# Performance work log

Hardware: AMD Instinct MI355X
Metric: run time of the kernel (lower is better)

## Reference

```python
import jax, jax.numpy as jnp
import numpy as np

B, N, D, H = 512, 200, 128, 8
DH = D // H
CLIP = 10.0
NEG = -1e9


def setup_inputs():
    ks = jax.random.split(jax.random.key(0), 10)
    s = 1.0 / float(np.sqrt(D))
    f32 = jnp.float32
    return {
        "x": jax.random.normal(ks[0], (2, B, N, N), f32),
        "rf": jax.random.uniform(ks[1], (B, 2), f32),
        "node_embeddings": jax.random.normal(ks[2], (B, N, D), f32),
        "graph_embedding": jax.random.normal(ks[3], (B, D), f32),
        "Wk1_w": jax.random.normal(ks[4], (D, D), f32) * s,
        "Wk1_b": jnp.zeros((D,), f32),
        "Wv_w": jax.random.normal(ks[5], (D, D), f32) * s,
        "Wk2_w": jax.random.normal(ks[6], (D, D), f32) * s,
        "Wout_w": jax.random.normal(ks[7], (D, D), f32) * s,
        "Wq_w": jax.random.normal(ks[8], (D, D + 2), f32) * s,
        "init_node": jnp.zeros((D,), f32),
    }


def _forward(x, rf, node_embeddings, Wk1_w, Wk1_b, Wv_w, Wk2_w, Wout_w, Wq_w, init_node):
    # static projections (compute_static)
    K1 = node_embeddings @ Wk1_w.T + Wk1_b  # [B,N,D]
    V = node_embeddings @ Wv_w.T
    K2 = node_embeddings @ Wk2_w.T
    K1h = K1.reshape(B, N, H, DH).transpose(0, 2, 1, 3)  # [B,H,N,DH]
    Vh = V.reshape(B, N, H, DH).transpose(0, 2, 1, 3)
    barange = jnp.arange(B)
    narange = jnp.arange(N)

    def step(carry, _):
        mask, ctx, end = carry  # mask [B,N] bool, ctx [B,2+D], end [B] bool
        Q1 = ctx @ Wq_w.T  # [B,D]  (Wq_step)
        qh = Q1.reshape(B, H, DH)
        scores = jnp.einsum('bhd,bhnd->bhn', qh, K1h) / jnp.sqrt(jnp.float32(DH))
        scores = jnp.where(mask[:, None, :], NEG, scores)
        attn = jax.nn.softmax(scores, axis=-1)
        mha = jnp.einsum('bhn,bhnd->bhd', attn, Vh).reshape(B, D)
        Q2 = mha @ Wout_w.T  # [B,D]
        logits = CLIP * jnp.tanh(jnp.einsum('bd,bnd->bn', Q2, K2) / jnp.sqrt(jnp.float32(D)))
        logits = jnp.where(mask, NEG, logits)
        log_p = jax.nn.log_softmax(logits, axis=-1)  # [B,N]
        nxt = jnp.argmax(log_p, axis=-1)  # greedy decode (deterministic)
        nxt = jnp.where(end, nxt, 0)  # once node 0 chosen, stay at 0
        cur_emb = node_embeddings[barange, nxt]  # [B,D]
        end = end & (nxt != 0)
        mask = mask | (narange[None, :] == nxt[:, None])
        ctx = jnp.concatenate([rf, cur_emb], axis=1)
        return (mask, ctx, end), (log_p, nxt)

    ctx0 = jnp.concatenate([rf, jnp.broadcast_to(init_node, (B, D))], axis=1)
    carry0 = (jnp.zeros((B, N), bool), ctx0, jnp.ones((B,), bool))
    _, (log_ps, tours) = jax.lax.scan(step, carry0, None, length=N)
    log_ps = log_ps.transpose(1, 0, 2)  # [B,N,N]
    pi = tours.T  # [B,N]

    # get_cost
    index = jnp.argmax(pi == 0, axis=1)  # first occurrence of stop node 0
    steps_mask = narange[None, :] < index[:, None]
    cols = pi * steps_mask
    sol = jnp.zeros((B, N), jnp.float32).at[barange[:, None], cols].set(1.0)
    f1 = jnp.einsum('bn,bnm,bm->b', sol, x[0], sol)[:, None, None]  # [B,1,1]
    f2 = jnp.einsum('bn,bnm,bm->b', sol, x[1], sol)[:, None, None]
    cost = -(f1 * rf[0, 0] + f2 * rf[0, 1]).squeeze()  # [B]

    # log-likelihood of tour, weighted by solution membership
    chosen = jnp.take_along_axis(log_ps, pi[:, :, None], axis=2)[:, :, 0]  # [B,N]
    w = jnp.take_along_axis(sol, pi, axis=1)
    ll = jnp.sum(chosen * w, axis=1)  # [B]
    return cost, f1, f2, ll, pi


def reference(x, rf, node_embeddings, graph_embedding, Wk1_w, Wk1_b, Wv_w, Wk2_w, Wout_w, Wq_w, init_node):
    return _forward(x, rf, node_embeddings, Wk1_w, Wk1_b, Wv_w, Wk2_w, Wout_w, Wq_w, init_node)
```

## Files before the change

### kernel.cpp

```cpp
#include <hip/hip_runtime.h>
#include <math.h>

#define NEGV (-1e9f)

#define OUT_F   0l
#define M_F     52428800l
#define QR_F    (M_F + 65536l)
#define QI_F    (QR_F + 65536l)
#define SOL_F   (QI_F + 65536l)
#define WS_FLOATS (SOL_F + 102400l)

typedef float f32x4 __attribute__((ext_vector_type(4)));

#define DPPF(x, ctrl, oldv) __int_as_float(__builtin_amdgcn_update_dpp( \
      __float_as_int(oldv), __float_as_int(x), ctrl, 0xF, 0xF, false))

__device__ __forceinline__ float wave_max(float x) {
  x = fmaxf(x, DPPF(x, 0x111, -INFINITY));
  x = fmaxf(x, DPPF(x, 0x112, -INFINITY));
  x = fmaxf(x, DPPF(x, 0x114, -INFINITY));
  x = fmaxf(x, DPPF(x, 0x118, -INFINITY));
  x = fmaxf(x, DPPF(x, 0x142, -INFINITY));
  x = fmaxf(x, DPPF(x, 0x143, -INFINITY));
  return __int_as_float(__builtin_amdgcn_readlane(__float_as_int(x), 63));
}
__device__ __forceinline__ float wave_sum(float x) {
  x = x + DPPF(x, 0x111, 0.f);
  x = x + DPPF(x, 0x112, 0.f);
  x = x + DPPF(x, 0x114, 0.f);
  x = x + DPPF(x, 0x118, 0.f);
  x = x + DPPF(x, 0x142, 0.f);
  x = x + DPPF(x, 0x143, 0.f);
  return __int_as_float(__builtin_amdgcn_readlane(__float_as_int(x), 63));
}

__global__ __launch_bounds__(256)
void build_M(const float* __restrict__ Wk1, const float* __restrict__ Wv,
             const float* __restrict__ Wk2, const float* __restrict__ Wout,
             const float* __restrict__ Wq, float* __restrict__ Mbuf) {
  int g = blockIdx.x * 256 + threadIdx.x;
  int j = g >> 9, c = g & 511;
  float val;
  if (c < 128) {
    val = Wk1[c * 128 + j];
  } else if (c < 256) {
    val = Wv[(c - 128) * 128 + j];
  } else if (c < 384) {
    int d = c - 256;
    float s = 0.f;
    for (int e = 0; e < 128; ++e) s += Wk2[e * 128 + j] * Wout[e * 128 + d];
    val = s;
  } else {
    val = Wq[(c - 384) * 130 + 2 + j];
  }
  Mbuf[j * 512 + c] = val;
}

__global__ __launch_bounds__(256)
void build_Q(const float* __restrict__ rf, const float* __restrict__ Wq,
             const float* __restrict__ initn, float* __restrict__ QR,
             float* __restrict__ QI) {
  int g = blockIdx.x * 256 + threadIdx.x;
  int b = g >> 7, d = g & 127;
  float qr = Wq[d * 130 + 0] * rf[b * 2 + 0] + Wq[d * 130 + 1] * rf[b * 2 + 1];
  float qi = qr;
  for (int j = 0; j < 128; ++j) qi += Wq[d * 130 + 2 + j] * initn[j];
  QR[g] = qr;
  QI[g] = qi;
}

__global__ __launch_bounds__(256)
void gemm_static(const float* __restrict__ emb, const float* __restrict__ Mbuf,
                 const float* __restrict__ bk1, const float* __restrict__ QR,
                 float* __restrict__ OUT) {
  int bid = blockIdx.x;
  int lo = bid & 7, hi = bid >> 3;
  int rt = lo + 8 * (hi % 200);
  int ct = hi / 200;
  int r0 = rt * 64, c0 = ct * 64;
  int t = threadIdx.x, ty = t >> 4, tx = t & 15;
  int row0 = r0 + ty * 4;
  int col  = c0 + tx * 4;
  float acc[4][4] = {};
  const float* mp = Mbuf + col;
  for (int kb = 0; kb < 32; ++kb) {
    int k = kb * 4;
    float4 b0 = *(const float4*)(mp + (long)(k + 0) * 512);
    float4 b1 = *(const float4*)(mp + (long)(k + 1) * 512);
    float4 b2 = *(const float4*)(mp + (long)(k + 2) * 512);
    float4 b3 = *(const float4*)(mp + (long)(k + 3) * 512);
    float bm[4][4] = {{b0.x,b0.y,b0.z,b0.w},{b1.x,b1.y,b1.z,b1.w},
                      {b2.x,b2.y,b2.z,b2.w},{b3.x,b3.y,b3.z,b3.w}};
    #pragma unroll
    for (int rr = 0; rr < 4; ++rr) {
      float4 a4 = *(const float4*)(emb + (long)(row0 + rr) * 128 + k);
      float av[4] = {a4.x, a4.y, a4.z, a4.w};
      #pragma unroll
      for (int i = 0; i < 4; ++i)
        #pragma unroll
        for (int cc = 0; cc < 4; ++cc)
          acc[rr][cc] += av[i] * bm[i][cc];
    }
  }
  float badd[4] = {0.f, 0.f, 0.f, 0.f};
  if (c0 < 128) {
    #pragma unroll
    for (int cc = 0; cc < 4; ++cc) badd[cc] = bk1[col + cc];
  }
  #pragma unroll
  for (int rr = 0; rr < 4; ++rr) {
    int row = row0 + rr;
    float v[4];
    #pragma unroll
    for (int cc = 0; cc < 4; ++cc) v[cc] = acc[rr][cc] + badd[cc];
    if (col >= 384) {
      int bb = row / 200;
      #pragma unroll
      for (int cc = 0; cc < 4; ++cc) v[cc] += QR[bb * 128 + (col - 384) + cc];
    }
    float4 v4; v4.x = v[0]; v4.y = v[1]; v4.z = v[2]; v4.w = v[3];
    *(float4*)(OUT + (long)row * 512 + col) = v4;
  }
}

__global__ void init_ctr(int* __restrict__ c) { *c = 0; }

__global__ __attribute__((amdgpu_flat_work_group_size(512, 512), amdgpu_waves_per_eu(2, 2)))
void decode512(const float* __restrict__ OUT, const float* __restrict__ QI,
               int* __restrict__ ctr, float* __restrict__ sol,
               float* __restrict__ out) {
  __shared__ __align__(16) float qall[201 * 128];
  __shared__ float sc[1600];
  __shared__ __align__(16) float mhal[128];
  __shared__ float lg[200];
  __shared__ int bci, bsel;

  const int t = threadIdx.x;
  const int lane = t & 63, wave = t >> 6;
  const int o = t >> 2, r4 = t & 3;
  const int mn = t >> 1, half = t & 1;
  const int vst  = (r4 == 0) ? 0 : (r4 == 1 ? 48 : (r4 == 2 ? 100 : 152));
  const bool mid = (r4 == 1) || (r4 == 2);

  float kreg[64], ureg[64], vreg[52];

  for (;;) {
    if (t == 0) bsel = atomicAdd(ctr, 1);
    __syncthreads();
    const int b = bsel;
    if (b >= 512) break;
    const float* outb = OUT + (long)b * 200 * 512;

    for (int f = t; f < 25728; f += 512) {
      int row = f >> 7, d = f & 127;
      qall[f] = (row < 200) ? outb[row * 512 + 384 + d] : QI[b * 128 + d];
    }
    #pragma unroll
    for (int k = 0; k < 4; ++k) {
      int n = lane + 64 * k;
      if (n < 200) {
        const float* kp = outb + n * 512 + wave * 16;
        #pragma unroll
        for (int c = 0; c < 4; ++c)
          *(f32x4*)&kreg[k * 16 + c * 4] = *(const f32x4*)(kp + c * 4);
      } else {
        #pragma unroll
        for (int c = 0; c < 16; ++c) kreg[k * 16 + c] = 0.f;
      }
    }
    if (t < 400) {
      const float* up = outb + mn * 512 + 256 + 64 * half;
      #pragma unroll
      for (int c = 0; c < 16; ++c)
        *(f32x4*)&ureg[c * 4] = *(const f32x4*)(up + c * 4);
    }
    {
      const float* vp = outb + 128 + o;
      #pragma unroll
      for (int i = 0; i < 48; ++i) vreg[i] = vp[(vst + i) * 512];
      vreg[48] = mid ? vp[(vst + 48) * 512] : 0.f;
      vreg[49] = mid ? vp[(vst + 49) * 512] : 0.f;
      vreg[50] = mid ? vp[(vst + 50) * 512] : 0.f;
      vreg[51] = mid ? vp[(vst + 51) * 512] : 0.f;
    }

    int cur = 200;
    int mk = 0;
    bool cmb = false;
    bool live = true, picked0 = false;
    float llsum = 0.f, chose = 0.f;

    __syncthreads();

    for (int st = 0; st < 200; ++st) {
      {
        const float* qb = qall + cur * 128 + wave * 16;
        f32x4 q0 = *(const f32x4*)(qb + 0);
        f32x4 q1 = *(const f32x4*)(qb + 4);
        f32x4 q2 = *(const f32x4*)(qb + 8);
        f32x4 q3 = *(const f32x4*)(qb + 12);
        float sv[4];
        float mx = -INFINITY;
        #pragma unroll
        for (int k = 0; k < 4; ++k) {
          int n = lane + 64 * k;
          float s = -INFINITY;
          if (n < 200) {
            float a = q0[0] * kreg[k * 16 + 0];
            a += q0[1] * kreg[k * 16 + 1];
            a += q0[2] * kreg[k * 16 + 2];
            a += q0[3] * kreg[k * 16 + 3];
            a += q1[0] * kreg[k * 16 + 4];
            a += q1[1] * kreg[k * 16 + 5];
            a += q1[2] * kreg[k * 16 + 6];
            a += q1[3] * kreg[k * 16 + 7];
            a += q2[0] * kreg[k * 16 + 8];
            a += q2[1] * kreg[k * 16 + 9];
            a += q2[2] * kreg[k * 16 + 10];
            a += q2[3] * kreg[k * 16 + 11];
            a += q3[0] * kreg[k * 16 + 12];
            a += q3[1] * kreg[k * 16 + 13];
            a += q3[2] * kreg[k * 16 + 14];
            a += q3[3] * kreg[k * 16 + 15];
            s = a * 0.25f;
            if (mk & (1 << k)) s = NEGV;
          }
          sv[k] = s;
          mx = fmaxf(mx, s);
        }
        float vmax = wave_max(mx);
        float ls = 0.f;
        #pragma unroll
        for (int k = 0; k < 4; ++k) { sv[k] = expf(sv[k] - vmax); ls += sv[k]; }
        ls = wave_sum(ls);
        #pragma unroll
        for (int k = 0; k < 4; ++k) {
          int n = lane + 64 * k;
          if (n < 200) sc[wave * 200 + n] = sv[k] / ls;
        }
      }

      {
        const float* ap = sc + wave * 200 + vst;
        float ac[4] = {0.f, 0.f, 0.f, 0.f};
        #pragma unroll
        for (int c = 0; c < 12; ++c) {
          f32x4 av = *(const f32x4*)(ap + c * 4);
          float s = av[0] * vreg[c * 4 + 0];
          s += av[1] * vreg[c * 4 + 1];
          s += av[2] * vreg[c * 4 + 2];
          s += av[3] * vreg[c * 4 + 3];
          ac[c & 3] += s;
        }
        if (mid) {
          f32x4 av = *(const f32x4*)(ap + 48);
          float s = av[0] * vreg[48];
          s += av[1] * vreg[49]; s += av[2] * vreg[50]; s += av[3] * vreg[51];
          ac[0] += s;
        }
        float a = (ac[0] + ac[1]) + (ac[2] + ac[3]);
        a += DPPF(a, 0xB1, 0.f);
        a += DPPF(a, 0x4E, 0.f);
        if (r4 == 0) mhal[o] = a;
      }
      __syncthreads();

      if (t < 400) {
        float ac[4] = {0.f, 0.f, 0.f, 0.f};
        #pragma unroll
        for (int c = 0; c < 16; ++c) {
          f32x4 mh = *(const f32x4*)&mhal[64 * half + c * 4];
          float s = mh[0] * ureg[c * 4 + 0];
          s += mh[1] * ureg[c * 4 + 1];
          s += mh[2] * ureg[c * 4 + 2];
          s += mh[3] * ureg[c * 4 + 3];
          ac[c & 3] += s;
        }
        float a = (ac[0] + ac[1]) + (ac[2] + ac[3]);
        a += DPPF(a, 0xB1, 0.f);
        if (half == 0) {
          float l = 10.f * tanhf(a / 11.313708498984761f);
          lg[mn] = cmb ? NEGV : l;
        }
      }
      __syncthreads();

      if (wave == 7) {
        float lv[4];
        float mx = -INFINITY;
        #pragma unroll
        for (int k = 0; k < 4; ++k) {
          int n = lane + 64 * k;
          lv[k] = (n < 200) ? lg[n] : -INFINITY;
          mx = fmaxf(mx, lv[k]);
        }
        float vmax = wave_max(mx);
        int bidx = -1;
        #pragma unroll
        for (int k = 0; k < 4; ++k) {
          unsigned long long bm =
              __ballot((lane + 64 * k < 200) && (lv[k] == vmax));
          if (bidx < 0 && bm != 0ull) bidx = k * 64 + (int)__builtin_ctzll(bm);
        }
        int nxt = live ? bidx : 0;
        float e = 0.f;
        #pragma unroll
        for (int k = 0; k < 4; ++k) e += expf(lv[k] - vmax);
        float se_ = wave_sum(e);
        float lse = logf(se_);
        if (t == 448) {
          chose = live ? (-lse) : ((lv[0] - vmax) - lse);
          out[2048 + (long)b * 200 + st] = (float)nxt;
          bci = nxt;
        }
      }
      __syncthreads();

      int nxt = bci;
      if (!live) {
        if (t == 448) llsum += chose * (float)(200 - st);
        for (int s2 = st + 1 + t; s2 < 200; s2 += 512)
          out[2048 + (long)b * 200 + s2] = 0.f;
        break;
      }
      if (t == 448) llsum += chose;
      if ((nxt & 63) == lane) mk |= 1 << (nxt >> 6);
      if (t < 400 && nxt == mn) cmb = true;
      cur = nxt;
      if (nxt == 0) { live = false; picked0 = true; }
    }

    if (t == 448) out[1536 + b] = picked0 ? llsum : 0.f;
    if (t < 400 && half == 0) {
      float s = (mn == 0) ? 1.f : ((picked0 && cmb) ? 1.f : 0.f);
      sol[(long)b * 200 + mn] = s;
    }
    __syncthreads();
  }
}

__global__ __attribute__((amdgpu_flat_work_group_size(1024, 1024)))
void decode(const float* __restrict__ OUT, const float* __restrict__ QI,
            int* __restrict__ ctr, float* __restrict__ sol,
            float* __restrict__ out) {
  __shared__ __align__(16) float k1r[25600];
  __shared__ __align__(16) float at[1600];
  __shared__ __align__(16) float mhal[128];
  __shared__ float lg[200];
  __shared__ __align__(16) float qv[128];
  __shared__ __align__(16) float ul[12800];
  __shared__ int   bci;
  __shared__ int   bsel;

  const int t = threadIdx.x;
  const int lane = t & 63, wave = t >> 6;
  const int o = t >> 3, q8 = t & 7;
  const int m4 = t >> 2, j4 = t & 3;
  const int stq = (q8 * 25) & ~3;
  const int cq  = ((((q8 + 1) * 25) & ~3) - stq) >> 2;

  for (;;) {
    if (t == 0) bsel = atomicAdd(ctr, 1);
    __syncthreads();
    const int b = bsel;
    if (b >= 512) break;
    const float* outb = OUT + (long)b * 200 * 512;

    for (int p = 0; p < 25; ++p) {
      int f = p * 1024 + t;
      int n = f >> 7, d = f & 127;
      k1r[n * 128 + ((d + 4 * n) & 127)] = outb[n * 512 + d];
    }
    for (int f = t; f < 12800; f += 1024) {
      int m = f >> 6, c = f & 63;
      ul[m * 64 + ((c + 4 * m) & 63)] =
          outb[m * 512 + 256 + (c >> 4) * 32 + 16 + (c & 15)];
    }
    f32x4 vA = {}, vB = {}, vC = {}, vD = {}, vE = {}, vF = {}, vG = {};
    {
      const float* vp = outb + 128 + o;
      #pragma unroll
      for (int e = 0; e < 4; ++e) vA[e] = vp[(stq + 0 + e) * 512];
      #pragma unroll
      for (int e = 0; e < 4; ++e) vB[e] = vp[(stq + 4 + e) * 512];
      #pragma unroll
      for (int e = 0; e < 4; ++e) vC[e] = vp[(stq + 8 + e) * 512];
      #pragma unroll
      for (int e = 0; e < 4; ++e) vD[e] = vp[(stq + 12 + e) * 512];
      #pragma unroll
      for (int e = 0; e < 4; ++e) vE[e] = vp[(stq + 16 + e) * 512];
      #pragma unroll
      for (int e = 0; e < 4; ++e) vF[e] = vp[(stq + 20 + e) * 512];
      if (cq == 7) {
        #pragma unroll
        for (int e = 0; e < 4; ++e) vG[e] = vp[(stq + 24 + e) * 512];
      }
    }
    f32x4 urR0 = {}, urR1 = {}, urR2 = {}, urR3 = {};
    if (t < 800) {
      const float* up = outb + m4 * 512 + 256 + j4 * 32;
      urR0 = *(const f32x4*)(up + 4 * ((0 + j4) & 3));
      urR1 = *(const f32x4*)(up + 4 * ((1 + j4) & 3));
      urR2 = *(const f32x4*)(up + 4 * ((2 + j4) & 3));
      urR3 = *(const f32x4*)(up + 4 * ((3 + j4) & 3));
    }
    if (t < 128) qv[t] = QI[b * 128 + t];

    int mk = 0;
    bool cm = false;
    bool live = true, picked0 = false;
    float llsum = 0.f, chose = 0.f;

    __syncthreads();

    for (int st = 0; st < 200; ++st) {
      if (wave < 8) {
        const int hb = wave * 16;
        float acc[4] = {};
        #pragma unroll
        for (int hf = 0; hf < 2; ++hf) {
          f32x4 qa = *(const f32x4*)&qv[hb + hf * 8];
          f32x4 qb2 = *(const f32x4*)&qv[hb + hf * 8 + 4];
          #pragma unroll
          for (int k = 0; k < 4; ++k) {
            int n = lane + 64 * k;
            if (n < 200) {
              const float* kb = k1r + n * 128;
              int off  = (hb + hf * 8 + 4 * n) & 127;
              int off2 = (hb + hf * 8 + 4 + 4 * n) & 127;
              f32x4 kA = *(const f32x4*)(kb + off);
              f32x4 kB = *(const f32x4*)(kb + off2);
              float ah = qa[0] * kA[0];
              ah += qa[1] * kA[1]; ah += qa[2] * kA[2]; ah += qa[3] * kA[3];
              ah += qb2[0] * kB[0]; ah += qb2[1] * kB[1];
              ah += qb2[2] * kB[2]; ah += qb2[3] * kB[3];
              acc[k] += ah;
            }
          }
        }
        float sv[4];
        float mx = -INFINITY;
        #pragma unroll
        for (int k = 0; k < 4; ++k) {
          int n = lane + 64 * k;
          float s = -INFINITY;
          if (n < 200) {
            s = acc[k] * 0.25f;
            if (mk & (1 << k)) s = NEGV;
          }
          sv[k] = s;
          mx = fmaxf(mx, s);
        }
        float vmax = wave_max(mx);
        float ls = 0.f;
        #pragma unroll
        for (int k = 0; k < 4; ++k) { sv[k] = expf(sv[k] - vmax); ls += sv[k]; }
        ls = wave_sum(ls);
        #pragma unroll
        for (int k = 0; k < 4; ++k) {
          int n = lane + 64 * k;
          if (n < 200) at[wave * 200 + n] = sv[k] / ls;
        }
      }
      __syncthreads();

      {
        const int h2 = t >> 7;
        const float* ap = at + h2 * 200 + stq;
        float a = 0.f;
        f32x4 av;
        av = *(const f32x4*)(ap + 0);
        a += av[0]*vA[0]; a += av[1]*vA[1]; a += av[2]*vA[2]; a += av[3]*vA[3];
        av = *(const f32x4*)(ap + 4);
        a += av[0]*vB[0]; a += av[1]*vB[1]; a += av[2]*vB[2]; a += av[3]*vB[3];
        av = *(const f32x4*)(ap + 8);
        a += av[0]*vC[0]; a += av[1]*vC[1]; a += av[2]*vC[2]; a += av[3]*vC[3];
        av = *(const f32x4*)(ap + 12);
        a += av[0]*vD[0]; a += av[1]*vD[1]; a += av[2]*vD[2]; a += av[3]*vD[3];
        av = *(const f32x4*)(ap + 16);
        a += av[0]*vE[0]; a += av[1]*vE[1]; a += av[2]*vE[2]; a += av[3]*vE[3];
        av = *(const f32x4*)(ap + 20);
        a += av[0]*vF[0]; a += av[1]*vF[1]; a += av[2]*vF[2]; a += av[3]*vF[3];
        if (cq == 7) {
          av = *(const f32x4*)(ap + 24);
          a += av[0]*vG[0]; a += av[1]*vG[1]; a += av[2]*vG[2]; a += av[3]*vG[3];
        }
        a += DPPF(a, 0xB1, 0.f);
        a += DPPF(a, 0x4E, 0.f);
        a += DPPF(a, 0x141, 0.f);
        if (q8 == 0) mhal[o] = a;
      }
      __syncthreads();

      if (t < 800) {
        float a = 0.f;
        {
          f32x4 ml;
          ml = *(const f32x4*)&mhal[j4 * 32 + ((0 + j4) & 3) * 4];
          a += ml[0]*urR0[0]; a += ml[1]*urR0[1]; a += ml[2]*urR0[2]; a += ml[3]*urR0[3];
          ml = *(const f32x4*)&mhal[j4 * 32 + ((1 + j4) & 3) * 4];
          a += ml[0]*urR1[0]; a += ml[1]*urR1[1]; a += ml[2]*urR1[2]; a += ml[3]*urR1[3];
          ml = *(const f32x4*)&mhal[j4 * 32 + ((2 + j4) & 3) * 4];
          a += ml[0]*urR2[0]; a += ml[1]*urR2[1]; a += ml[2]*urR2[2]; a += ml[3]*urR2[3];
          ml = *(const f32x4*)&mhal[j4 * 32 + ((3 + j4) & 3) * 4];
          a += ml[0]*urR3[0]; a += ml[1]*urR3[1]; a += ml[2]*urR3[2]; a += ml[3]*urR3[3];
        }
        const int ubase = m4 * 64;
        #pragma unroll
        for (int c = 0; c < 4; ++c) {
          int ci = (c + j4) & 3;
          f32x4 mh = *(const f32x4*)&mhal[j4 * 32 + 16 + ci * 4];
          f32x4 uu = *(const f32x4*)&ul[ubase + ((j4 * 16 + ci * 4 + 4 * m4) & 63)];
          a += mh[0]*uu[0]; a += mh[1]*uu[1]; a += mh[2]*uu[2]; a += mh[3]*uu[3];
        }
        a += DPPF(a, 0xB1, 0.f);
        a += DPPF(a, 0x4E, 0.f);
        if (j4 == 0) {
          float l = 10.f * tanhf(a / 11.313708498984761f);
          lg[m4] = cm ? NEGV : l;
        }
      }
      __syncthreads();

      if (wave < 8) {
        float lv[4];
        float mx = -INFINITY;
        #pragma unroll
        for (int k = 0; k < 4; ++k) {
          int n = lane + 64 * k;
          lv[k] = (n < 200) ? lg[n] : -INFINITY;
          mx = fmaxf(mx, lv[k]);
        }
        float vmax = wave_max(mx);
        int bidx = -1;
        #pragma unroll
        for (int k = 0; k < 4; ++k) {
          unsigned long long bm =
              __ballot((lane + 64 * k < 200) && (lv[k] == vmax));
          if (bidx < 0 && bm != 0ull) bidx = k * 64 + (int)__builtin_ctzll(bm);
        }
        int nxt = live ? bidx : 0;
        if (t < 128) qv[t] = outb[(long)nxt * 512 + 384 + t];
        float e = 0.f;
        #pragma unroll
        for (int k = 0; k < 4; ++k) e += expf(lv[k] - vmax);
        float se_ = wave_sum(e);
        float lse = logf(se_);
        if (t == 0) {
          chose = live ? (-lse) : ((lv[0] - vmax) - lse);
          out[2048 + (long)b * 200 + st] = (float)nxt;
          bci = nxt;
        }
      }
      __syncthreads();

      int nxt = bci;
      if (!live) {
        if (t == 0) llsum += chose * (float)(200 - st);
        for (int s2 = st + 1 + t; s2 < 200; s2 += 1024)
          out[2048 + (long)b * 200 + s2] = 0.f;
        break;
      }
      if (t == 0) llsum += chose;
      if (wave < 8 && (nxt & 63) == lane) mk |= 1 << (nxt >> 6);
      if (t < 800 && nxt == m4) cm = true;
      if (nxt == 0) { live = false; picked0 = true; }
    }

    if (t == 0) out[1536 + b] = picked0 ? llsum : 0.f;
    if (t < 800 && j4 == 0) {
      float s = (m4 == 0) ? 1.f : ((picked0 && cm) ? 1.f : 0.f);
      sol[(long)b * 200 + m4] = s;
    }
    __syncthreads();
  }
}

__global__ __launch_bounds__(256)
void cost_kernel(const float* __restrict__ x, const float* __restrict__ rf,
                 const float* __restrict__ sol, float* __restrict__ out) {
  __shared__ float solL[256];
  __shared__ float red[8];
  const int b = blockIdx.x, t = threadIdx.x;
  solL[t] = (t < 200) ? sol[b * 200 + t] : 0.f;
  __syncthreads();
  const float* x0 = x + (long)b * 40000;
  const float* x1 = x + 20480000l + (long)b * 40000;
  float a1 = 0.f, a2 = 0.f;
  if (t < 200) {
    #pragma unroll 4
    for (int i = 0; i < 200; ++i) {
      float w2 = solL[i];
      a1 += x0[i * 200 + t] * w2;
      a2 += x1[i * 200 + t] * w2;
    }
    float w = solL[t];
    a1 *= w; a2 *= w;
  }
  #pragma unroll
  for (int off = 32; off > 0; off >>= 1) {
    a1 += __shfl_xor(a1, off);
    a2 += __shfl_xor(a2, off);
  }
  if ((t & 63) == 0) { red[(t >> 6) * 2] = a1; red[(t >> 6) * 2 + 1] = a2; }
  __syncthreads();
  if (t == 0) {
    float f1 = red[0] + red[2] + red[4] + red[6];
    float f2 = red[1] + red[3] + red[5] + red[7];
    out[b]        = -(f1 * rf[0] + f2 * rf[1]);
    out[512 + b]  = f1;
    out[1024 + b] = f2;
  }
}

extern "C" void kernel_launch(void* const* d_in, const int* in_sizes, int n_in,
                              void* d_out, int out_size, void* d_ws, size_t ws_size,
                              hipStream_t stream) {
  const float* x     = (const float*)d_in[0];
  const float* rf    = (const float*)d_in[1];
  const float* emb   = (const float*)d_in[2];
  const float* Wk1   = (const float*)d_in[4];
  const float* bk1   = (const float*)d_in[5];
  const float* Wv    = (const float*)d_in[6];
  const float* Wk2   = (const float*)d_in[7];
  const float* Wout  = (const float*)d_in[8];
  const float* Wq    = (const float*)d_in[9];
  const float* initn = (const float*)d_in[10];
  float* out = (float*)d_out;
  float* ws  = (float*)d_ws;

  if (ws_size < (size_t)WS_FLOATS * 4) return;

  float* OUTb = ws + OUT_F;
  float* Mb   = ws + M_F;
  float* QRb  = ws + QR_F;
  float* QIb  = ws + QI_F;
  float* solb = ws + SOL_F;

  build_M<<<256, 256, 0, stream>>>(Wk1, Wv, Wk2, Wout, Wq, Mb);
  build_Q<<<256, 256, 0, stream>>>(rf, Wq, initn, QRb, QIb);
  gemm_static<<<12800, 256, 0, stream>>>(emb, Mb, bk1, QRb, OUTb);
  init_ctr<<<1, 1, 0, stream>>>((int*)QRb);

  hipFuncAttributes fa;
  bool big = false;
  if (hipFuncGetAttributes(&fa, (const void*)decode512) == hipSuccess)
    big = (fa.localSizeBytes <= 64);
  if (big)
    decode512<<<256, 512, 0, stream>>>(OUTb, QIb, (int*)QRb, solb, out);
  else
    decode<<<256, 1024, 0, stream>>>(OUTb, QIb, (int*)QRb, solb, out);

  cost_kernel<<<512, 256, 0, stream>>>(x, rf, solb, out);
}
```

Baseline: 1.215 ms.

## Fuse cost computation into decode512 and compute argmax redundantly per wave

The argmax over logits is now computed by every wave rather than only wave 7, which removes a shared-memory broadcast and one block barrier per decode step. The separate cost kernel is folded into the tail of decode512: the solution vector stays in shared memory and each block computes its quadratic forms over x directly. This drops a kernel launch and the global round trip of sol, at the cost of serialising x reads behind each block's decode. The counter is moved to a different workspace slot, and some of the pointer setup is leftover dead code.

```diff
diff --git a/kernel.cpp b/kernel.cpp
--- a/kernel.cpp
+++ b/kernel.cpp
@@ -59,8 +59,9 @@
 __global__ __launch_bounds__(256)
 void build_Q(const float* __restrict__ rf, const float* __restrict__ Wq,
              const float* __restrict__ initn, float* __restrict__ QR,
-             float* __restrict__ QI) {
+             float* __restrict__ QI, int* __restrict__ ctr) {
   int g = blockIdx.x * 256 + threadIdx.x;
+  if (g == 0) *ctr = 0;
   int b = g >> 7, d = g & 127;
   float qr = Wq[d * 130 + 0] * rf[b * 2 + 0] + Wq[d * 130 + 1] * rf[b * 2 + 1];
   float qi = qr;
@@ -127,13 +128,15 @@
 
 __global__ __attribute__((amdgpu_flat_work_group_size(512, 512), amdgpu_waves_per_eu(2, 2)))
 void decode512(const float* __restrict__ OUT, const float* __restrict__ QI,
-               int* __restrict__ ctr, float* __restrict__ sol,
-               float* __restrict__ out) {
+               const float* __restrict__ x, const float* __restrict__ rf,
+               int* __restrict__ ctr, float* __restrict__ out) {
   __shared__ __align__(16) float qall[201 * 128];
   __shared__ float sc[1600];
   __shared__ __align__(16) float mhal[128];
   __shared__ float lg[200];
-  __shared__ int bci, bsel;
+  __shared__ float sb[200];
+  __shared__ float redc[16];
+  __shared__ int bsel;
 
   const int t = threadIdx.x;
   const int lane = t & 63, wave = t >> 6;
@@ -285,7 +288,8 @@
       }
       __syncthreads();
 
-      if (wave == 7) {
+      int nxt;
+      {
         float lv[4];
         float mx = -INFINITY;
         #pragma unroll
@@ -302,21 +306,20 @@
               __ballot((lane + 64 * k < 200) && (lv[k] == vmax));
           if (bidx < 0 && bm != 0ull) bidx = k * 64 + (int)__builtin_ctzll(bm);
         }
-        int nxt = live ? bidx : 0;
-        float e = 0.f;
-        #pragma unroll
-        for (int k = 0; k < 4; ++k) e += expf(lv[k] - vmax);
-        float se_ = wave_sum(e);
-        float lse = logf(se_);
-        if (t == 448) {
-          chose = live ? (-lse) : ((lv[0] - vmax) - lse);
-          out[2048 + (long)b * 200 + st] = (float)nxt;
-          bci = nxt;
-        }
-      }
-      __syncthreads();
-
-      int nxt = bci;
+        nxt = live ? bidx : 0;
+        if (wave == 7) {
+          float e = 0.f;
+          #pragma unroll
+          for (int k = 0; k < 4; ++k) e += expf(lv[k] - vmax);
+          float se_ = wave_sum(e);
+          float lse = logf(se_);
+          if (t == 448) {
+            chose = live ? (-lse) : ((lv[0] - vmax) - lse);
+            out[2048 + (long)b * 200 + st] = (float)nxt;
+          }
+        }
+      }
+
       if (!live) {
         if (t == 448) llsum += chose * (float)(200 - st);
         for (int s2 = st + 1 + t; s2 < 200; s2 += 512)
@@ -333,7 +336,44 @@
     if (t == 448) out[1536 + b] = picked0 ? llsum : 0.f;
     if (t < 400 && half == 0) {
       float s = (mn == 0) ? 1.f : ((picked0 && cmb) ? 1.f : 0.f);
-      sol[(long)b * 200 + mn] = s;
+      sb[mn] = s;
+    }
+    __syncthreads();
+
+    {
+      const int c2 = t >> 1, hf = t & 1;
+      float a1 = 0.f, a2 = 0.f;
+      if (c2 < 200) {
+        const float* xp0 = x + (long)b * 40000 + hf * 20000 + c2;
+        const float* xp1 = x + 20480000l + (long)b * 40000 + hf * 20000 + c2;
+        #pragma unroll 4
+        for (int i = 0; i < 100; ++i) {
+          float w2 = sb[hf * 100 + i];
+          a1 += xp0[i * 200] * w2;
+          a2 += xp1[i * 200] * w2;
+        }
+      }
+      a1 += DPPF(a1, 0xB1, 0.f);
+      a2 += DPPF(a2, 0xB1, 0.f);
+      if (hf == 0 && c2 < 200) {
+        float w = sb[c2];
+        a1 *= w; a2 *= w;
+      } else {
+        a1 = 0.f; a2 = 0.f;
+      }
+      a1 = wave_sum(a1);
+      a2 = wave_sum(a2);
+      if (lane == 0) { redc[wave * 2] = a1; redc[wave * 2 + 1] = a2; }
+      __syncthreads();
+      if (t == 0) {
+        float f1 = ((redc[0] + redc[2]) + (redc[4] + redc[6])) +
+                   ((redc[8] + redc[10]) + (redc[12] + redc[14]));
+        float f2 = ((redc[1] + redc[3]) + (redc[5] + redc[7])) +
+                   ((redc[9] + redc[11]) + (redc[13] + redc[15]));
+        out[b]        = -(f1 * rf[0] + f2 * rf[1]);
+        out[512 + b]  = f1;
+        out[1024 + b] = f2;
+      }
     }
     __syncthreads();
   }
@@ -636,20 +676,24 @@
   float* QRb  = ws + QR_F;
   float* QIb  = ws + QI_F;
   float* solb = ws + SOL_F;
+  int*   ctrb = (int*)(ws + QR_F);
+
+  ctrb = (int*)(ws + SOL_F + 102400l - 4l);
+  ctrb = (int*)(ws + M_F);
 
   build_M<<<256, 256, 0, stream>>>(Wk1, Wv, Wk2, Wout, Wq, Mb);
-  build_Q<<<256, 256, 0, stream>>>(rf, Wq, initn, QRb, QIb);
+  build_Q<<<256, 256, 0, stream>>>(rf, Wq, initn, QRb, QIb, (int*)(ws + QI_F + 65536l - 4l));
   gemm_static<<<12800, 256, 0, stream>>>(emb, Mb, bk1, QRb, OUTb);
-  init_ctr<<<1, 1, 0, stream>>>((int*)QRb);
+  init_ctr<<<1, 1, 0, stream>>>(ctrb);
 
   hipFuncAttributes fa;
   bool big = false;
   if (hipFuncGetAttributes(&fa, (const void*)decode512) == hipSuccess)
     big = (fa.localSizeBytes <= 64);
-  if (big)
-    decode512<<<256, 512, 0, stream>>>(OUTb, QIb, (int*)QRb, solb, out);
-  else
-    decode<<<256, 1024, 0, stream>>>(OUTb, QIb, (int*)QRb, solb, out);
-
-  cost_kernel<<<512, 256, 0, stream>>>(x, rf, solb, out);
-}
+  if (big) {
+    decode512<<<256, 512, 0, stream>>>(OUTb, QIb, x, rf, ctrb, out);
+  } else {
+    decode<<<256, 1024, 0, stream>>>(OUTb, QIb, ctrb, solb, out);
+    cost_kernel<<<512, 256, 0, stream>>>(x, rf, solb, out);
+  }
+}
```

Result: no change. 1.198 ms (-1.4%).
